# Performance work log

Hardware: AMD Instinct MI355X
Metric: run time of the kernel (lower is better)

## Reference

```python
import jax, jax.numpy as jnp
import numpy as np
from jax import lax

DIM = 1024
D_STATE = 64
D_CONV = 4
EXPAND = 2
HEADDIM = 64
D_INNER = EXPAND * DIM            # 2048
NHEADS = D_INNER // HEADDIM       # 32
NGROUPS = 1
CONV_DIM = D_INNER + 2 * NGROUPS * D_STATE      # 2176
D_IN_PROJ = 2 * D_INNER + 2 * NGROUPS * D_STATE + NHEADS  # 4256
BATCH, SEQLEN = 2, 4096
EPS = 1e-5


def setup_inputs() -> dict:
    key = jax.random.key(0)
    ks = jax.random.split(key, 10)
    X = jax.random.normal(ks[0], (BATCH, SEQLEN, DIM), dtype=jnp.float32)
    in_proj_w = jax.random.normal(ks[1], (D_IN_PROJ, DIM), dtype=jnp.float32) * 0.02
    conv_w = jax.random.normal(ks[2], (CONV_DIM, 1, D_CONV), dtype=jnp.float32) * 0.2
    conv_b = jax.random.normal(ks[3], (CONV_DIM,), dtype=jnp.float32) * 0.02
    dt_bias = jax.random.normal(ks[4], (NHEADS,), dtype=jnp.float32) * 0.5 - 2.0
    A_log = jnp.log(jax.random.uniform(ks[5], (NHEADS,), minval=1.0, maxval=16.0))
    D = jax.random.normal(ks[6], (NHEADS,), dtype=jnp.float32)
    norm_w = jnp.ones((D_INNER,), dtype=jnp.float32)
    out_proj_w = jax.random.normal(ks[7], (DIM, D_INNER), dtype=jnp.float32) * 0.02
    to_h_w = jax.random.normal(ks[8], (2 * DIM, DIM), dtype=jnp.float32) * 0.02
    return dict(X=X, in_proj_w=in_proj_w, conv_w=conv_w, conv_b=conv_b,
                dt_bias=dt_bias, A_log=A_log, D=D, norm_w=norm_w,
                out_proj_w=out_proj_w, to_h_w=to_h_w)


def _silu(x):
    return x * jax.nn.sigmoid(x)


def _mamba2(X, in_proj_w, conv_w, conv_b, dt_bias, A_log, D, norm_w, out_proj_w):
    Bsz, L, _ = X.shape
    zxbcdt = jnp.einsum('bld,ed->ble', X, in_proj_w)  # (B,L,D_IN_PROJ)
    z = zxbcdt[..., :D_INNER]
    xBC = zxbcdt[..., D_INNER:D_INNER + CONV_DIM]
    dt_raw = zxbcdt[..., D_INNER + CONV_DIM:]
    dt = jax.nn.softplus(dt_raw + dt_bias)  # (B,L,H)

    # causal depthwise conv over time, then silu
    xc = jnp.transpose(xBC, (0, 2, 1))                       # (B,C,L)
    xc = jnp.pad(xc, ((0, 0), (0, 0), (D_CONV - 1, 0)))
    xc = lax.conv_general_dilated(xc, conv_w, window_strides=(1,), padding='VALID',
                                  dimension_numbers=('NCH', 'OIH', 'NCH'),
                                  feature_group_count=CONV_DIM)
    xc = xc + conv_b[None, :, None]
    xBC = _silu(jnp.transpose(xc, (0, 2, 1)))                # (B,L,C)

    x = xBC[..., :D_INNER].reshape(Bsz, L, NHEADS, HEADDIM)  # (B,L,H,P)
    Bm = xBC[..., D_INNER:D_INNER + D_STATE]                 # (B,L,N) ngroups=1
    Cm = xBC[..., D_INNER + D_STATE:]                        # (B,L,N)

    A = -jnp.exp(A_log)                                      # (H,)

    def step(h, inp):
        dt_t, B_t, C_t, x_t = inp   # (B,H), (B,N), (B,N), (B,H,P)
        dA = jnp.exp(dt_t * A)                               # (B,H)
        h = h * dA[..., None, None] + jnp.einsum('bh,bhp,bn->bhpn', dt_t, x_t, B_t)
        y_t = jnp.einsum('bhpn,bn->bhp', h, C_t)
        return h, y_t

    h0 = jnp.zeros((Bsz, NHEADS, HEADDIM, D_STATE), dtype=X.dtype)
    xs = (jnp.moveaxis(dt, 1, 0), jnp.moveaxis(Bm, 1, 0),
          jnp.moveaxis(Cm, 1, 0), jnp.moveaxis(x, 1, 0))
    _, ys = lax.scan(step, h0, xs)                           # (L,B,H,P)
    y = jnp.moveaxis(ys, 0, 1) + x * D[None, None, :, None]  # skip term
    y = y.reshape(Bsz, L, D_INNER)

    # gated RMSNorm: rmsnorm(y * silu(z)) * weight
    y = y * _silu(z)
    y = y * lax.rsqrt(jnp.mean(y * y, axis=-1, keepdims=True) + EPS) * norm_w
    return jnp.einsum('bld,ed->ble', y, out_proj_w)          # (B,L,DIM)


def reference(X, in_proj_w, conv_w, conv_b, dt_bias, A_log, D, norm_w, out_proj_w, to_h_w):
    H = _mamba2(X, in_proj_w, conv_w, conv_b, dt_bias, A_log, D, norm_w, out_proj_w)
    HKV = jnp.einsum('bld,ed->ble', H, to_h_w)               # (B,L,2*DIM)
    HK, HV = HKV[..., :DIM], HKV[..., DIM:]
    return (HK, HV)
```

## Files before the change

kernel.cpp:

```cpp
#include <hip/hip_runtime.h>
#include <hip/hip_bf16.h>
#include <math.h>

#define B_       2
#define L_       4096
#define DIM_     1024
#define DINNER_  2048
#define DSTATE_  64
#define NH_      32
#define HD_      64
#define CONVDIM_ 2176
#define DIP_     4256
#define M_       (B_*L_)
#define XRW_     2208
#define NC_      64

typedef __attribute__((ext_vector_type(8))) short short8;
typedef __attribute__((ext_vector_type(4))) float floatx4;
typedef __hip_bfloat16 bf16;

__device__ __forceinline__ float bf2f(unsigned short u) {
    unsigned int v = ((unsigned int)u) << 16;
    return __builtin_bit_cast(float, v);
}
__device__ __forceinline__ unsigned short f2bf(float f) {
    unsigned int x = __builtin_bit_cast(unsigned int, f);
    unsigned int lsb = (x >> 16) & 1u;
    x += 0x7fffu + lsb;
    return (unsigned short)(x >> 16);
}
__device__ __forceinline__ void storeo(bf16* p, float v) {
    *reinterpret_cast<unsigned short*>(p) = f2bf(v);
}
__device__ __forceinline__ void storeo(float* p, float v) { *p = v; }

__device__ __forceinline__ void gl2lds16(const bf16* g, short* lds) {
    __builtin_amdgcn_global_load_lds(
        (const __attribute__((address_space(1))) void*)g,
        (__attribute__((address_space(3))) void*)lds, 16, 0, 0);
}

__global__ __launch_bounds__(256) void cast_f32_bf16_k(
    const float* __restrict__ src, bf16* __restrict__ dst)
{
    size_t i0 = ((size_t)blockIdx.x * 256 + threadIdx.x) * 8;
    uint4 a = *reinterpret_cast<const uint4*>(src + i0);
    uint4 b = *reinterpret_cast<const uint4*>(src + i0 + 4);
    unsigned int w0 = (unsigned int)f2bf(__builtin_bit_cast(float, a.x)) |
                      ((unsigned int)f2bf(__builtin_bit_cast(float, a.y)) << 16);
    unsigned int w1 = (unsigned int)f2bf(__builtin_bit_cast(float, a.z)) |
                      ((unsigned int)f2bf(__builtin_bit_cast(float, a.w)) << 16);
    unsigned int w2 = (unsigned int)f2bf(__builtin_bit_cast(float, b.x)) |
                      ((unsigned int)f2bf(__builtin_bit_cast(float, b.y)) << 16);
    unsigned int w3 = (unsigned int)f2bf(__builtin_bit_cast(float, b.z)) |
                      ((unsigned int)f2bf(__builtin_bit_cast(float, b.w)) << 16);
    *reinterpret_cast<uint4*>(reinterpret_cast<unsigned short*>(dst) + i0) =
        make_uint4(w0, w1, w2, w3);
}

__global__ __launch_bounds__(256) void cast_transpose_k(
    const float* __restrict__ src, bf16* __restrict__ dst, int R, int C)
{
    __shared__ unsigned short t[64][72];
    int nct = C >> 6;
    int r0 = (blockIdx.x / nct) << 6;
    int c0 = (blockIdx.x % nct) << 6;
    int tr = threadIdx.x >> 2;
    int tc = (threadIdx.x & 3) << 4;
    const float* s = src + (size_t)(r0 + tr) * C + c0 + tc;
#pragma unroll
    for (int k = 0; k < 16; k += 4) {
        float4 v = *reinterpret_cast<const float4*>(s + k);
        t[tr][tc + k + 0] = f2bf(v.x);
        t[tr][tc + k + 1] = f2bf(v.y);
        t[tr][tc + k + 2] = f2bf(v.z);
        t[tr][tc + k + 3] = f2bf(v.w);
    }
    __syncthreads();
    unsigned short* d = (unsigned short*)dst + (size_t)(c0 + tr) * R + r0 + tc;
    unsigned int ww[8];
#pragma unroll
    for (int q = 0; q < 8; q++)
        ww[q] = (unsigned int)t[tc + 2*q][tr] | ((unsigned int)t[tc + 2*q + 1][tr] << 16);
    *reinterpret_cast<uint4*>(d)     = make_uint4(ww[0], ww[1], ww[2], ww[3]);
    *reinterpret_cast<uint4*>(d + 8) = make_uint4(ww[4], ww[5], ww[6], ww[7]);
}

template <typename TO>
__global__ __launch_bounds__(256) void gemm_bt16(
    const bf16* __restrict__ A, const bf16* __restrict__ W,
    TO* __restrict__ outA, TO* __restrict__ outB,
    int M, int N, int K, int split, int strideA, int strideB)
{
    __shared__ short As[128*64];
    __shared__ short Ws[128*64];
    const int tid  = threadIdx.x;
    const int m0   = blockIdx.y * 128;
    const int n0   = blockIdx.x * 128;
    const int wave = tid >> 6;
    const int lane = tid & 63;
    const int wm   = (wave >> 1) * 64;
    const int wn   = (wave & 1) * 64;
    const int ln   = lane & 15;
    const int quad = lane >> 4;
    const int lr   = lane >> 3;
    const int lc   = (lane & 7) * 8;

    floatx4 acc[4][4];
#pragma unroll
    for (int i = 0; i < 4; i++)
#pragma unroll
        for (int j = 0; j < 4; j++) acc[i][j] = (floatx4){0.f, 0.f, 0.f, 0.f};

    for (int k0 = 0; k0 < K; k0 += 64) {
#pragma unroll
        for (int it = 0; it < 4; it++) {
            int ig = wave * 4 + it;
            gl2lds16(A + (size_t)(m0 + ig * 8 + lr) * K + k0 + lc, &As[ig * 512]);
            gl2lds16(W + (size_t)(n0 + ig * 8 + lr) * K + k0 + lc, &Ws[ig * 512]);
        }
        __syncthreads();
#pragma unroll
        for (int kk = 0; kk < 64; kk += 32) {
            short8 af[4], bfv[4];
#pragma unroll
            for (int i = 0; i < 4; i++)
                af[i] = *reinterpret_cast<const short8*>(&As[(wm + i * 16 + ln) * 64 + kk + quad * 8]);
#pragma unroll
            for (int j = 0; j < 4; j++)
                bfv[j] = *reinterpret_cast<const short8*>(&Ws[(wn + j * 16 + ln) * 64 + kk + quad * 8]);
#pragma unroll
            for (int i = 0; i < 4; i++)
#pragma unroll
                for (int j = 0; j < 4; j++)
                    acc[i][j] = __builtin_amdgcn_mfma_f32_16x16x32_bf16(af[i], bfv[j], acc[i][j], 0, 0, 0);
        }
        __syncthreads();
    }

#pragma unroll
    for (int i = 0; i < 4; i++)
#pragma unroll
        for (int j = 0; j < 4; j++)
#pragma unroll
            for (int r = 0; r < 4; r++) {
                int grow = m0 + wm + i * 16 + quad * 4 + r;
                int gcol = n0 + wn + j * 16 + ln;
                if (gcol < N) {
                    if (gcol < split)
                        storeo(outA + (size_t)grow * strideA + gcol, acc[i][j][r]);
                    else
                        storeo(outB + (size_t)grow * strideB + (gcol - split), acc[i][j][r]);
                }
            }
}

template <typename TO>
__global__ __launch_bounds__(512, 2) void gemm256(
    const bf16* __restrict__ Ag, const bf16* __restrict__ Wg,
    TO* __restrict__ outA, TO* __restrict__ outB,
    int M, int N, int K, int split, int strideA, int strideB, int nbx)
{
    __shared__ short lds[65536];

    const int tid  = threadIdx.x;
    const int wave = tid >> 6;
    const int lane = tid & 63;
    const int ln   = lane & 15;
    const int quad = lane >> 4;
    const int wr   = wave >> 2;
    const int wc   = wave & 3;
    const int bh   = wc >> 1;
    const int wcl  = wc & 1;
    const int xorv = (ln & 7) << 4;

    int nwg  = gridDim.x;
    int orig = blockIdx.x;
    int wg   = ((nwg & 7) == 0) ? ((orig & 7) * (nwg >> 3) + (orig >> 3)) : orig;
    const int bx = wg % nbx;
    const int by = wg / nbx;
    const int m0 = by * 256;
    const int n0 = bx * 256;

    int lo0 = tid * 16;
    int lo1 = 8192 + tid * 16;
    int so0 = lo0 ^ (((lo0 >> 7) & 7) << 4);
    int so1 = lo1 ^ (((lo1 >> 7) & 7) << 4);
    const int srow0 = so0 >> 7, scol0 = (so0 & 127) >> 1;
    const int srow1 = so1 >> 7, scol1 = (so1 & 127) >> 1;

#define STG_A(bufb, h, kc) do {                                               \
    short* dst_ = &lds[((bufb)*2 + (h)) * 8192 + wave * 512];                 \
    gl2lds16(Ag + (size_t)(m0 + (h)*128 + srow0) * K + (kc) + scol0, dst_);   \
    gl2lds16(Ag + (size_t)(m0 + (h)*128 + srow1) * K + (kc) + scol1, dst_ + 4096); \
} while (0)
#define STG_B(bufb, h, kc) do {                                               \
    short* dst_ = &lds[32768 + ((bufb)*2 + (h)) * 8192 + wave * 512];         \
    gl2lds16(Wg + (size_t)(n0 + (h)*128 + srow0) * K + (kc) + scol0, dst_);   \
    gl2lds16(Wg + (size_t)(n0 + (h)*128 + srow1) * K + (kc) + scol1, dst_ + 4096); \
} while (0)

#define RD_A(qi) do {                                                         \
    const char* Ab_ = (const char*)&lds[(cur*2 + wr) * 8192];                 \
    _Pragma("unroll") for (int i = 0; i < 4; i++)                             \
    _Pragma("unroll") for (int ks = 0; ks < 2; ks++)                          \
        af[i][ks] = *reinterpret_cast<const short8*>(                         \
            Ab_ + ((((qi)*64 + i*16 + ln)*128 + ks*64 + quad*16) ^ xorv));    \
} while (0)
#define RD_B(qj, BV) do {                                                     \
    const char* Bb_ = (const char*)&lds[32768 + (cur*2 + bh) * 8192];         \
    _Pragma("unroll") for (int j = 0; j < 2; j++)                             \
    _Pragma("unroll") for (int ks = 0; ks < 2; ks++)                          \
        BV[j][ks] = *reinterpret_cast<const short8*>(                         \
            Bb_ + (((wcl*64 + (qj)*32 + j*16 + ln)*128 + ks*64 + quad*16) ^ xorv)); \
} while (0)

#define MMA(qi, qj, BV) do {                                                  \
    _Pragma("unroll") for (int i = 0; i < 4; i++)                             \
    _Pragma("unroll") for (int j = 0; j < 2; j++)                             \
    _Pragma("unroll") for (int ks = 0; ks < 2; ks++)                          \
        acc[(qi)*4+i][(qj)*2+j] = __builtin_amdgcn_mfma_f32_16x16x32_bf16(    \
            af[i][ks], BV[j][ks], acc[(qi)*4+i][(qj)*2+j], 0, 0, 0);          \
} while (0)

    floatx4 acc[8][4];
#pragma unroll
    for (int i = 0; i < 8; i++)
#pragma unroll
        for (int j = 0; j < 4; j++) acc[i][j] = (floatx4){0.f, 0.f, 0.f, 0.f};

    const int NT = K >> 6;

    STG_A(0, 0, 0); STG_A(0, 1, 0);
    STG_B(0, 0, 0); STG_B(0, 1, 0);
    asm volatile("s_waitcnt vmcnt(0)" ::: "memory");
    __builtin_amdgcn_s_barrier();
    __builtin_amdgcn_sched_barrier(0);

    short8 af[4][2], bf0[2][2], bf1[2][2];

    for (int t = 0; t < NT; ++t) {
        const int cur = t & 1, nxt = cur ^ 1;
        const int kc  = (t + 1) << 6;
        const bool pf = (t + 1 < NT);

        RD_A(0);
        RD_B(0, bf0);
        RD_B(1, bf1);

        if (pf) {
            STG_A(nxt, 0, kc); STG_A(nxt, 1, kc);
            STG_B(nxt, 0, kc); STG_B(nxt, 1, kc);
        }

        __builtin_amdgcn_s_setprio(1);
        MMA(0, 0, bf0);
        MMA(0, 1, bf1);
        RD_A(1);
        MMA(1, 1, bf1);
        MMA(1, 0, bf0);
        __builtin_amdgcn_s_setprio(0);

        if (pf) { asm volatile("s_waitcnt vmcnt(0)" ::: "memory"); }
        __builtin_amdgcn_s_barrier();
        __builtin_amdgcn_sched_barrier(0);
    }

#undef STG_A
#undef STG_B
#undef RD_A
#undef RD_B
#undef MMA

#pragma unroll
    for (int qi = 0; qi < 2; qi++)
#pragma unroll
    for (int i = 0; i < 4; i++)
#pragma unroll
    for (int qj = 0; qj < 2; qj++)
#pragma unroll
    for (int j = 0; j < 2; j++)
#pragma unroll
    for (int r = 0; r < 4; r++) {
        int grow = m0 + wr*128 + qi*64 + i*16 + quad*4 + r;
        int gcol = n0 + wc*64 + qj*32 + j*16 + ln;
        float v = acc[qi*4+i][qj*2+j][r];
        if (gcol < N) {
            if (gcol < split)
                storeo(outA + (size_t)grow * strideA + gcol, v);
            else
                storeo(outB + (size_t)grow * strideB + (gcol - split), v);
        }
    }
}

__global__ __launch_bounds__(256) void conv_all_k(
    const bf16* __restrict__ xr, const float* __restrict__ cw,
    const float* __restrict__ cb, bf16* __restrict__ xc)
{
    int idx = blockIdx.x * 256 + threadIdx.x;
    int row = idx / 272;
    int ch0 = (idx - row * 272) * 8;
    int t   = row & (L_ - 1);
    const unsigned short* xru = (const unsigned short*)xr;
    uint4 rv[4];
#pragma unroll
    for (int j = 0; j < 4; j++) {
        rv[j] = make_uint4(0u, 0u, 0u, 0u);
        if (t + j - 3 >= 0)
            rv[j] = *reinterpret_cast<const uint4*>(xru + (size_t)(row + j - 3) * XRW_ + ch0);
    }
    unsigned int ow[4];
#pragma unroll
    for (int pair = 0; pair < 4; pair++) {
        unsigned short o2[2];
#pragma unroll
        for (int k = 0; k < 2; k++) {
            int cc = pair * 2 + k;
            float a = cb[ch0 + cc];
#pragma unroll
            for (int j = 0; j < 4; j++) {
                unsigned int w32 = (&rv[j].x)[cc >> 1];
                unsigned short u = (cc & 1) ? (unsigned short)(w32 >> 16)
                                            : (unsigned short)(w32 & 0xffffu);
                a = fmaf(bf2f(u), cw[(ch0 + cc) * 4 + j], a);
            }
            o2[k] = f2bf(a / (1.f + __expf(-a)));
        }
        ow[pair] = (unsigned int)o2[0] | ((unsigned int)o2[1] << 16);
    }
    *reinterpret_cast<uint4*>((unsigned short*)xc + (size_t)row * CONVDIM_ + ch0) =
        make_uint4(ow[0], ow[1], ow[2], ow[3]);
}

__global__ __launch_bounds__(256) void dt_k(
    const bf16* __restrict__ xr, const float* __restrict__ dtb, float* __restrict__ dtf)
{
    int idx = blockIdx.x * 256 + threadIdx.x;
    int h  = idx & (NH_ - 1);
    int ml = idx >> 5;
    float v = bf2f(((const unsigned short*)xr)[(size_t)ml * XRW_ + 2176 + h]) + dtb[h];
    dtf[idx] = fmaxf(v, 0.f) + log1pf(__expf(-fabsf(v)));
}

__global__ __launch_bounds__(256) void chunk_intra_k(
    const bf16* __restrict__ xc, const float* __restrict__ dtf,
    const float* __restrict__ A_log, const float* __restrict__ Dp,
    bf16* __restrict__ Yg, float* __restrict__ Sg, float* __restrict__ Eg)
{
    __shared__ short Bst[64*72];
    __shared__ short Cst[64*72];
    __shared__ short xsM[64*72];
    __shared__ short xT [64*72];
    __shared__ short BwT[64*72];
    __shared__ float dts[64], cums[64], wS[64];

    const int tid  = threadIdx.x;
    const int bid  = blockIdx.x;
    const int h    = bid & 31;
    const int bc   = bid >> 5;
    const int c    = bc & 63;
    const int b    = bc >> 6;
    const int xch0 = h * 64;
    const unsigned short* xcu = (const unsigned short*)xc;

    const float Ah = -__expf(A_log[h]);
    const float Dh = Dp[h];

    for (int q = tid; q < 1536; q += 256) {
        int sel = q >> 9;
        int qq  = q & 511;
        int r = qq >> 3, c8 = (qq & 7) * 8;
        size_t ro = (size_t)(b * L_ + c * 64 + r) * CONVDIM_;
        if (sel == 0)
            *reinterpret_cast<uint4*>(&Bst[r*72 + c8]) =
                *reinterpret_cast<const uint4*>(xcu + ro + 2048 + c8);
        else if (sel == 1)
            *reinterpret_cast<uint4*>(&Cst[r*72 + c8]) =
                *reinterpret_cast<const uint4*>(xcu + ro + 2112 + c8);
        else
            *reinterpret_cast<uint4*>(&xsM[r*72 + c8]) =
                *reinterpret_cast<const uint4*>(xcu + ro + xch0 + c8);
    }
    if (tid < 64) dts[tid] = dtf[(size_t)(b * L_ + c * 64 + tid) * NH_ + h];
    __syncthreads();

    if (tid == 0) {
        float cc = 0.f;
        for (int t = 0; t < 64; t++) { cc += dts[t] * Ah; cums[t] = cc; }
    }
    __syncthreads();
    if (tid < 64) wS[tid] = __expf(cums[63] - cums[tid]) * dts[tid];
    if (tid == 0) Eg[bid] = __expf(cums[63]);
    __syncthreads();

    for (int q = tid; q < 4096; q += 256) {
        int s = q & 63, ch = q >> 6;
        xT [ch*72 + s] = xsM[s*72 + ch];
        BwT[ch*72 + s] = (short)f2bf(bf2f((unsigned short)Bst[s*72 + ch]) * wS[s]);
    }
    __syncthreads();

    const int wave = tid >> 6, lane = tid & 63;
    const int ln = lane & 15, quad = lane >> 4;
    const int wm = (wave >> 1) * 32, wn = (wave & 1) * 32;

    floatx4 accG[2][2];
#pragma unroll
    for (int i = 0; i < 2; i++)
#pragma unroll
        for (int j = 0; j < 2; j++) accG[i][j] = (floatx4){0.f,0.f,0.f,0.f};
#pragma unroll
    for (int kk = 0; kk < 64; kk += 32) {
        short8 af[2], bfv[2];
#pragma unroll
        for (int i = 0; i < 2; i++)
            af[i] = *reinterpret_cast<const short8*>(&Cst[(wm + i*16 + ln)*72 + kk + quad*8]);
#pragma unroll
        for (int j = 0; j < 2; j++)
            bfv[j] = *reinterpret_cast<const short8*>(&Bst[(wn + j*16 + ln)*72 + kk + quad*8]);
#pragma unroll
        for (int i = 0; i < 2; i++)
#pragma unroll
            for (int j = 0; j < 2; j++)
                accG[i][j] = __builtin_amdgcn_mfma_f32_16x16x32_bf16(af[i], bfv[j], accG[i][j], 0,0,0);
    }
    __syncthreads();
#pragma unroll
    for (int i = 0; i < 2; i++)
#pragma unroll
        for (int j = 0; j < 2; j++)
#pragma unroll
            for (int r = 0; r < 4; r++) {
                int t = wm + i*16 + quad*4 + r;
                int s = wn + j*16 + ln;
                float v = (s <= t) ? __expf(cums[t] - cums[s]) * dts[s] * accG[i][j][r] : 0.f;
                xsM[t*72 + s] = (short)f2bf(v);
            }
    __syncthreads();

    floatx4 accY[2][2];
#pragma unroll
    for (int i = 0; i < 2; i++)
#pragma unroll
        for (int j = 0; j < 2; j++) accY[i][j] = (floatx4){0.f,0.f,0.f,0.f};
#pragma unroll
    for (int kk = 0; kk < 64; kk += 32) {
        short8 af[2], bfv[2];
#pragma unroll
        for (int i = 0; i < 2; i++)
            af[i] = *reinterpret_cast<const short8*>(&xsM[(wm + i*16 + ln)*72 + kk + quad*8]);
#pragma unroll
        for (int j = 0; j < 2; j++)
            bfv[j] = *reinterpret_cast<const short8*>(&xT[(wn + j*16 + ln)*72 + kk + quad*8]);
#pragma unroll
        for (int i = 0; i < 2; i++)
#pragma unroll
            for (int j = 0; j < 2; j++)
                accY[i][j] = __builtin_amdgcn_mfma_f32_16x16x32_bf16(af[i], bfv[j], accY[i][j], 0,0,0);
    }
    unsigned short* Yu = (unsigned short*)Yg;
#pragma unroll
    for (int i = 0; i < 2; i++)
#pragma unroll
        for (int j = 0; j < 2; j++)
#pragma unroll
            for (int r = 0; r < 4; r++) {
                int t = wm + i*16 + quad*4 + r;
                int p = wn + j*16 + ln;
                float yv = accY[i][j][r] + Dh * bf2f((unsigned short)xT[p*72 + t]);
                Yu[(size_t)(b*L_ + c*64 + t)*DINNER_ + xch0 + p] = f2bf(yv);
            }

    floatx4 accS[2][2];
#pragma unroll
    for (int i = 0; i < 2; i++)
#pragma unroll
        for (int j = 0; j < 2; j++) accS[i][j] = (floatx4){0.f,0.f,0.f,0.f};
#pragma unroll
    for (int kk = 0; kk < 64; kk += 32) {
        short8 af[2], bfv[2];
#pragma unroll
        for (int i = 0; i < 2; i++)
            af[i] = *reinterpret_cast<const short8*>(&xT[(wm + i*16 + ln)*72 + kk + quad*8]);
#pragma unroll
        for (int j = 0; j < 2; j++)
            bfv[j] = *reinterpret_cast<const short8*>(&BwT[(wn + j*16 + ln)*72 + kk + quad*8]);
#pragma unroll
        for (int i = 0; i < 2; i++)
#pragma unroll
            for (int j = 0; j < 2; j++)
                accS[i][j] = __builtin_amdgcn_mfma_f32_16x16x32_bf16(af[i], bfv[j], accS[i][j], 0,0,0);
    }
#pragma unroll
    for (int i = 0; i < 2; i++)
#pragma unroll
        for (int j = 0; j < 2; j++)
#pragma unroll
            for (int r = 0; r < 4; r++) {
                int p = wm + i*16 + quad*4 + r;
                int n = wn + j*16 + ln;
                Sg[(size_t)bid * 4096 + p*64 + n] = accS[i][j][r];
            }
}

__global__ __launch_bounds__(256) void chunk_state_k(
    float* __restrict__ Sg, const float* __restrict__ Eg)
{
    int g  = blockIdx.x * 1024 + threadIdx.x * 4;
    int bh = g >> 12;
    int b  = bh >> 5, h = bh & 31;
    int e  = g & 4095;
    float4 run = make_float4(0.f, 0.f, 0.f, 0.f);
    for (int c = 0; c < NC_; c++) {
        int bid = (b * 64 + c) * 32 + h;
        size_t idx = (size_t)bid * 4096 + e;
        float4 s = *reinterpret_cast<float4*>(&Sg[idx]);
        float  E = Eg[bid];
        *reinterpret_cast<float4*>(&Sg[idx]) = run;
        run.x = run.x * E + s.x;
        run.y = run.y * E + s.y;
        run.z = run.z * E + s.z;
        run.w = run.w * E + s.w;
    }
}

__global__ __launch_bounds__(256) void chunk_inter_k(
    const bf16* __restrict__ xc, const float* __restrict__ Sg,
    const float* __restrict__ dtf, const float* __restrict__ A_log,
    bf16* __restrict__ Yg)
{
    __shared__ short Cst[64*72];
    __shared__ short hpT[64*72];
    __shared__ float dts[64], cums[64], wcumL[64];

    const int tid = threadIdx.x;
    const int bid = blockIdx.x;
    const int h   = bid & 31;
    const int bc  = bid >> 5;
    const int c   = bc & 63;
    const int b   = bc >> 6;
    const unsigned short* xcu = (const unsigned short*)xc;

    const float Ah = -__expf(A_log[h]);

    for (int q = tid; q < 512; q += 256) {
        int r = q >> 3, c8 = (q & 7) * 8;
        *reinterpret_cast<uint4*>(&Cst[r*72 + c8]) =
            *reinterpret_cast<const uint4*>(xcu + (size_t)(b*L_ + c*64 + r)*CONVDIM_ + 2112 + c8);
    }
    for (int q = tid; q < 1024; q += 256) {
        int p = q >> 4, n4 = (q & 15) * 4;
        float4 v = *reinterpret_cast<const float4*>(&Sg[(size_t)bid * 4096 + p*64 + n4]);
        unsigned int lo = (unsigned int)f2bf(v.x) | ((unsigned int)f2bf(v.y) << 16);
        unsigned int hi = (unsigned int)f2bf(v.z) | ((unsigned int)f2bf(v.w) << 16);
        *reinterpret_cast<uint2*>(&hpT[p*72 + n4]) = make_uint2(lo, hi);
    }
    if (tid < 64) dts[tid] = dtf[(size_t)(b*L_ + c*64 + tid) * NH_ + h];
    __syncthreads();
    if (tid == 0) {
        float cc = 0.f;
        for (int t = 0; t < 64; t++) { cc += dts[t] * Ah; cums[t] = cc; }
    }
    __syncthreads();
    if (tid < 64) wcumL[tid] = __expf(cums[tid]);
    __syncthreads();

    const int wave = tid >> 6, lane = tid & 63;
    const int ln = lane & 15, quad = lane >> 4;
    const int wm = (wave >> 1) * 32, wn = (wave & 1) * 32;

    floatx4 acc[2][2];
#pragma unroll
    for (int i = 0; i < 2; i++)
#pragma unroll
        for (int j = 0; j < 2; j++) acc[i][j] = (floatx4){0.f,0.f,0.f,0.f};
#pragma unroll
    for (int kk = 0; kk < 64; kk += 32) {
        short8 af[2], bfv[2];
#pragma unroll
        for (int i = 0; i < 2; i++)
            af[i] = *reinterpret_cast<const short8*>(&Cst[(wm + i*16 + ln)*72 + kk + quad*8]);
#pragma unroll
        for (int j = 0; j < 2; j++)
            bfv[j] = *reinterpret_cast<const short8*>(&hpT[(wn + j*16 + ln)*72 + kk + quad*8]);
#pragma unroll
        for (int i = 0; i < 2; i++)
#pragma unroll
            for (int j = 0; j < 2; j++)
                acc[i][j] = __builtin_amdgcn_mfma_f32_16x16x32_bf16(af[i], bfv[j], acc[i][j], 0,0,0);
    }
    unsigned short* Yu = (unsigned short*)Yg;
#pragma unroll
    for (int i = 0; i < 2; i++)
#pragma unroll
        for (int j = 0; j < 2; j++)
#pragma unroll
            for (int r = 0; r < 4; r++) {
                int t = wm + i*16 + quad*4 + r;
                int p = wn + j*16 + ln;
                size_t idx = (size_t)(b*L_ + c*64 + t)*DINNER_ + h*64 + p;
                float yv = bf2f(Yu[idx]) + wcumL[t] * acc[i][j][r];
                Yu[idx] = f2bf(yv);
            }
}

__global__ __launch_bounds__(256) void gate_norm_k(
    bf16* __restrict__ y, const bf16* __restrict__ zbuf, const float* __restrict__ nw)
{
    __shared__ float red[4];
    int row = blockIdx.x;
    int tid = threadIdx.x;
    unsigned short* yy = (unsigned short*)y;
    const unsigned short* zz = (const unsigned short*)zbuf;

    uint4 yv = *reinterpret_cast<uint4*>(&yy[(size_t)row * DINNER_ + tid * 8]);
    uint4 zv = *reinterpret_cast<const uint4*>(&zz[(size_t)row * DINNER_ + tid * 8]);
    unsigned int yw[4] = {yv.x, yv.y, yv.z, yv.w};
    unsigned int zw[4] = {zv.x, zv.y, zv.z, zv.w};
    float g[8];
    float ss = 0.f;
#pragma unroll
    for (int q = 0; q < 4; q++) {
        float y0 = bf2f((unsigned short)(yw[q] & 0xffffu)), y1 = bf2f((unsigned short)(yw[q] >> 16));
        float z0 = bf2f((unsigned short)(zw[q] & 0xffffu)), z1 = bf2f((unsigned short)(zw[q] >> 16));
        float g0 = y0 * (z0 / (1.f + __expf(-z0)));
        float g1 = y1 * (z1 / (1.f + __expf(-z1)));
        g[q * 2] = g0; g[q * 2 + 1] = g1;
        ss += g0 * g0 + g1 * g1;
    }
#pragma unroll
    for (int o = 1; o < 64; o <<= 1) ss += __shfl_xor(ss, o);
    if ((tid & 63) == 0) red[tid >> 6] = ss;
    __syncthreads();
    float tot = red[0] + red[1] + red[2] + red[3];
    float rinv = rsqrtf(tot * (1.f / DINNER_) + 1e-5f);

    unsigned int ow[4];
#pragma unroll
    for (int q = 0; q < 4; q++) {
        float w0 = nw[tid * 8 + q * 2];
        float w1 = nw[tid * 8 + q * 2 + 1];
        unsigned short o0 = f2bf(g[q * 2] * rinv * w0);
        unsigned short o1 = f2bf(g[q * 2 + 1] * rinv * w1);
        ow[q] = (unsigned int)o0 | ((unsigned int)o1 << 16);
    }
    *reinterpret_cast<uint4*>(&yy[(size_t)row * DINNER_ + tid * 8]) =
        make_uint4(ow[0], ow[1], ow[2], ow[3]);
}


extern "C" void kernel_launch(void* const* d_in, const int* in_sizes, int n_in,
                              void* d_out, int out_size, void* d_ws, size_t ws_size,
                              hipStream_t stream)
{
    const float* X    = (const float*)d_in[0];
    const float* Wip  = (const float*)d_in[1];
    const float* cw   = (const float*)d_in[2];
    const float* cb   = (const float*)d_in[3];
    const float* dtb  = (const float*)d_in[4];
    const float* Alog = (const float*)d_in[5];
    const float* Dp   = (const float*)d_in[6];
    const float* nw   = (const float*)d_in[7];
    const float* Wop  = (const float*)d_in[8];
    const float* Wth  = (const float*)d_in[9];
    float* out = (float*)d_out;

    char* ws = (char*)d_ws;
    bf16*  zbuf = (bf16*) (ws);
    bf16*  WopT = (bf16*) (ws);
    bf16*  Wthb = (bf16*) (ws + 4194304);
    bf16*  Wc   = (bf16*) (ws + 8388608);
    bf16*  xr   = (bf16*) (ws + 33554432);
    bf16*  Yg   = (bf16*) (ws + 33554432);
    bf16*  xc   = (bf16*) (ws + 69730304);
    bf16*  Xb   = (bf16*) (ws + 69730304);
    bf16*  Wipb = (bf16*) (ws + 69730304 + 16777216);
    float* dtf  = (float*)(ws + 105381888);
    float* Eg   = (float*)(ws + 106430464);
    float* Sg   = (float*)d_out;

    dim3 blk(256);
    dim3 blk512(512);

    cast_f32_bf16_k<<<(M_ * DIM_) / 2048, blk, 0, stream>>>(X, Xb);
    cast_f32_bf16_k<<<(DIP_ * DIM_) / 2048, blk, 0, stream>>>(Wip, Wipb);

    gemm256<bf16><<<dim3(17 * 32), blk512, 0, stream>>>(
        Xb, Wipb, zbuf, xr, M_, DIP_, DIM_, DINNER_, DINNER_, XRW_, 17);

    dt_k<<<(M_ * NH_) / 256, blk, 0, stream>>>(xr, dtb, dtf);
    conv_all_k<<<(M_ * 272) / 256, blk, 0, stream>>>(xr, cw, cb, xc);

    chunk_intra_k<<<B_ * NC_ * NH_, blk, 0, stream>>>(
        xc, dtf, Alog, Dp, Yg, Sg, Eg);
    chunk_state_k<<<256, blk, 0, stream>>>(Sg, Eg);
    chunk_inter_k<<<B_ * NC_ * NH_, blk, 0, stream>>>(xc, Sg, dtf, Alog, Yg);

    gate_norm_k<<<M_, blk, 0, stream>>>(Yg, zbuf, nw);

    cast_transpose_k<<<(1024/64) * (2048/64), blk, 0, stream>>>(Wop, WopT, 1024, 2048);
    cast_f32_bf16_k<<<(DINNER_ * DIM_) / 2048, blk, 0, stream>>>(Wth, Wthb);
    gemm_bt16<bf16><<<dim3(16, 16), blk, 0, stream>>>(
        Wthb, WopT, Wc, Wc, DINNER_, DINNER_, DIM_, DINNER_, DINNER_, DINNER_);

    gemm256<float><<<dim3(8 * 32), blk512, 0, stream>>>(
        Yg, Wc, out, out + (size_t)M_ * DIM_, M_, DINNER_, DINNER_, DIM_, DIM_, DIM_, 8);
}
```

Baseline: 467.7 us.

## Switch gemm256 to triple-buffered K=32 stages with prefetch distance two

The 256x256 GEMM main loop now walks K in 32-wide steps and keeps three LDS stages instead of two 64-wide ones. Loads are issued two iterations ahead with vmcnt(4), so global-to-LDS traffic overlaps more compute and the loop waits less at each barrier. The swizzled LDS layout, staging offsets and fragment-offset tables are rebuilt for the 32-wide stages, and LDS use drops from 128KB to 96KB. In exchange each iteration does half the MFMA work per barrier, so there are twice as many barriers, and the address-offset arrays add register pressure.

```diff
diff --git a/kernel.cpp b/kernel.cpp
--- a/kernel.cpp
+++ b/kernel.cpp
@@ -161,7 +161,7 @@
     TO* __restrict__ outA, TO* __restrict__ outB,
     int M, int N, int K, int split, int strideA, int strideB, int nbx)
 {
-    __shared__ short lds[65536];
+    __shared__ short lds[49152];
 
     const int tid  = threadIdx.x;
     const int wave = tid >> 6;
@@ -172,7 +172,6 @@
     const int wc   = wave & 3;
     const int bh   = wc >> 1;
     const int wcl  = wc & 1;
-    const int xorv = (ln & 7) << 4;
 
     int nwg  = gridDim.x;
     int orig = blockIdx.x;
@@ -182,46 +181,33 @@
     const int m0 = by * 256;
     const int n0 = bx * 256;
 
-    int lo0 = tid * 16;
-    int lo1 = 8192 + tid * 16;
-    int so0 = lo0 ^ (((lo0 >> 7) & 7) << 4);
-    int so1 = lo1 ^ (((lo1 >> 7) & 7) << 4);
-    const int srow0 = so0 >> 7, scol0 = (so0 & 127) >> 1;
-    const int srow1 = so1 >> 7, scol1 = (so1 & 127) >> 1;
-
-#define STG_A(bufb, h, kc) do {                                               \
-    short* dst_ = &lds[((bufb)*2 + (h)) * 8192 + wave * 512];                 \
-    gl2lds16(Ag + (size_t)(m0 + (h)*128 + srow0) * K + (kc) + scol0, dst_);   \
-    gl2lds16(Ag + (size_t)(m0 + (h)*128 + srow1) * K + (kc) + scol1, dst_ + 4096); \
-} while (0)
-#define STG_B(bufb, h, kc) do {                                               \
-    short* dst_ = &lds[32768 + ((bufb)*2 + (h)) * 8192 + wave * 512];         \
-    gl2lds16(Wg + (size_t)(n0 + (h)*128 + srow0) * K + (kc) + scol0, dst_);   \
-    gl2lds16(Wg + (size_t)(n0 + (h)*128 + srow1) * K + (kc) + scol1, dst_ + 4096); \
-} while (0)
-
-#define RD_A(qi) do {                                                         \
-    const char* Ab_ = (const char*)&lds[(cur*2 + wr) * 8192];                 \
-    _Pragma("unroll") for (int i = 0; i < 4; i++)                             \
-    _Pragma("unroll") for (int ks = 0; ks < 2; ks++)                          \
-        af[i][ks] = *reinterpret_cast<const short8*>(                         \
-            Ab_ + ((((qi)*64 + i*16 + ln)*128 + ks*64 + quad*16) ^ xorv));    \
-} while (0)
-#define RD_B(qj, BV) do {                                                     \
-    const char* Bb_ = (const char*)&lds[32768 + (cur*2 + bh) * 8192];         \
-    _Pragma("unroll") for (int j = 0; j < 2; j++)                             \
-    _Pragma("unroll") for (int ks = 0; ks < 2; ks++)                          \
-        BV[j][ks] = *reinterpret_cast<const short8*>(                         \
-            Bb_ + (((wcl*64 + (qj)*32 + j*16 + ln)*128 + ks*64 + quad*16) ^ xorv)); \
-} while (0)
-
-#define MMA(qi, qj, BV) do {                                                  \
-    _Pragma("unroll") for (int i = 0; i < 4; i++)                             \
-    _Pragma("unroll") for (int j = 0; j < 2; j++)                             \
-    _Pragma("unroll") for (int ks = 0; ks < 2; ks++)                          \
-        acc[(qi)*4+i][(qj)*2+j] = __builtin_amdgcn_mfma_f32_16x16x32_bf16(    \
-            af[i][ks], BV[j][ks], acc[(qi)*4+i][(qj)*2+j], 0, 0, 0);          \
-} while (0)
+    {
+    }
+    const int su   = tid >> 3;
+    const int ssl  = (tid & 7) ^ (su & 7);
+    const int srow = (su << 1) | (ssl >> 2);
+    const int scol = (ssl & 3) << 3;
+
+    int aoff[8], boff[4];
+#pragma unroll
+    for (int i = 0; i < 8; i++) {
+        int row = i * 16 + ln;
+        aoff[i] = ((row >> 1) << 7) +
+                  (((((row & 1) << 2) | quad) ^ ((row >> 1) & 7)) << 4);
+    }
+#pragma unroll
+    for (int j = 0; j < 4; j++) {
+        int row = wcl * 64 + j * 16 + ln;
+        boff[j] = ((row >> 1) << 7) +
+                  (((((row & 1) << 2) | quad) ^ ((row >> 1) & 7)) << 4);
+    }
+
+#define STG_A(slot, h, kc) \
+    gl2lds16(Ag + (size_t)(m0 + (h)*128 + srow) * K + (kc) + scol, \
+             &lds[(slot)*8192 + (h)*4096 + wave*512])
+#define STG_B(slot, h, kc) \
+    gl2lds16(Wg + (size_t)(n0 + (h)*128 + srow) * K + (kc) + scol, \
+             &lds[24576 + (slot)*8192 + (h)*4096 + wave*512])
 
     floatx4 acc[8][4];
 #pragma unroll
@@ -229,62 +215,68 @@
 #pragma unroll
         for (int j = 0; j < 4; j++) acc[i][j] = (floatx4){0.f, 0.f, 0.f, 0.f};
 
-    const int NT = K >> 6;
-
-    STG_A(0, 0, 0); STG_A(0, 1, 0);
-    STG_B(0, 0, 0); STG_B(0, 1, 0);
-    asm volatile("s_waitcnt vmcnt(0)" ::: "memory");
+    const int NT = K >> 5;
+
+    STG_A(0, 0, 0);  STG_A(0, 1, 0);  STG_B(0, 0, 0);  STG_B(0, 1, 0);
+    STG_A(1, 0, 32); STG_A(1, 1, 32); STG_B(1, 0, 32); STG_B(1, 1, 32);
+    asm volatile("s_waitcnt vmcnt(4)" ::: "memory");
     __builtin_amdgcn_s_barrier();
     __builtin_amdgcn_sched_barrier(0);
 
-    short8 af[4][2], bf0[2][2], bf1[2][2];
+    const char* ldsb = (const char*)lds;
+    short8 af[8], bfv[4];
+    int cur = 0, s2 = 2;
 
     for (int t = 0; t < NT; ++t) {
-        const int cur = t & 1, nxt = cur ^ 1;
-        const int kc  = (t + 1) << 6;
-        const bool pf = (t + 1 < NT);
-
-        RD_A(0);
-        RD_B(0, bf0);
-        RD_B(1, bf1);
-
-        if (pf) {
-            STG_A(nxt, 0, kc); STG_A(nxt, 1, kc);
-            STG_B(nxt, 0, kc); STG_B(nxt, 1, kc);
+        if (t + 2 < NT) {
+            const int kc = (t + 2) << 5;
+            STG_A(s2, 0, kc); STG_A(s2, 1, kc);
+            STG_B(s2, 0, kc); STG_B(s2, 1, kc);
         }
 
+        const char* Ab = ldsb + cur * 16384 + wr * 8192;
+        const char* Bb = ldsb + 49152 + cur * 16384 + bh * 8192;
+#pragma unroll
+        for (int i = 0; i < 8; i++)
+            af[i] = *reinterpret_cast<const short8*>(Ab + aoff[i]);
+#pragma unroll
+        for (int j = 0; j < 4; j++)
+            bfv[j] = *reinterpret_cast<const short8*>(Bb + boff[j]);
+
         __builtin_amdgcn_s_setprio(1);
-        MMA(0, 0, bf0);
-        MMA(0, 1, bf1);
-        RD_A(1);
-        MMA(1, 1, bf1);
-        MMA(1, 0, bf0);
+#pragma unroll
+        for (int i = 0; i < 8; i++)
+#pragma unroll
+            for (int j = 0; j < 4; j++)
+                acc[i][j] = __builtin_amdgcn_mfma_f32_16x16x32_bf16(
+                    af[i], bfv[j], acc[i][j], 0, 0, 0);
         __builtin_amdgcn_s_setprio(0);
 
-        if (pf) { asm volatile("s_waitcnt vmcnt(0)" ::: "memory"); }
-        __builtin_amdgcn_s_barrier();
-        __builtin_amdgcn_sched_barrier(0);
+        if (t + 1 < NT) {
+            if (t + 2 < NT) {
+                asm volatile("s_waitcnt vmcnt(4)" ::: "memory");
+            } else {
+                asm volatile("s_waitcnt vmcnt(0)" ::: "memory");
+            }
+            __builtin_amdgcn_s_barrier();
+            __builtin_amdgcn_sched_barrier(0);
+        }
+        cur = (cur == 2) ? 0 : cur + 1;
+        s2  = (s2  == 2) ? 0 : s2  + 1;
     }
 
 #undef STG_A
 #undef STG_B
-#undef RD_A
-#undef RD_B
-#undef MMA
-
-#pragma unroll
-    for (int qi = 0; qi < 2; qi++)
-#pragma unroll
-    for (int i = 0; i < 4; i++)
-#pragma unroll
-    for (int qj = 0; qj < 2; qj++)
-#pragma unroll
-    for (int j = 0; j < 2; j++)
+
+#pragma unroll
+    for (int i = 0; i < 8; i++)
+#pragma unroll
+    for (int j = 0; j < 4; j++)
 #pragma unroll
     for (int r = 0; r < 4; r++) {
-        int grow = m0 + wr*128 + qi*64 + i*16 + quad*4 + r;
-        int gcol = n0 + wc*64 + qj*32 + j*16 + ln;
-        float v = acc[qi*4+i][qj*2+j][r];
+        int grow = m0 + wr*128 + i*16 + quad*4 + r;
+        int gcol = n0 + wc*64 + j*16 + ln;
+        float v = acc[i][j][r];
         if (gcol < N) {
             if (gcol < split)
                 storeo(outA + (size_t)grow * strideA + gcol, v);
```

After: 487.5 us. 1.04x slower.
